# Kernel tuning notes

Measured on AMD Instinct MI355X. Metric: run time of the kernel, lower is better.

Reference implementation:

```python
import jax, jax.numpy as jnp
import numpy as np

N_CLASSES = 2  # FS-MOL binary labels


def setup_inputs() -> dict:
    key = jax.random.key(0)
    k1, k2, k3 = jax.random.split(key, 3)
    Ns, Nq, d = 512, 16384, 512
    support_features = jax.random.normal(k1, (Ns, d), dtype=jnp.float32)
    support_labels = jax.random.randint(k2, (Ns,), 0, N_CLASSES, dtype=jnp.int64)
    query_features = jax.random.normal(k3, (Nq, d), dtype=jnp.float32)
    return {
        "support_features": support_features,
        "support_labels": support_labels,
        "query_features": query_features,
    }


def _cov(x):
    # rowvar=False covariance of [N, d] -> [d, d], matching _estimate_cov
    xc = x - jnp.mean(x, axis=0, keepdims=True)
    return (xc.T @ xc) / (x.shape[0] - 1)


def reference(support_features, support_labels, query_features):
    d = support_features.shape[1]
    dt = support_features.dtype
    task_cov = _cov(support_features)          # [d, d]
    reg = jnp.asarray(0.1, dt) * jnp.eye(d, dtype=dt)

    def per_class(c):
        mask = (support_labels == c).astype(dt)            # [Ns]
        n = mask.sum()                                      # scalar count
        mean = (mask[:, None] * support_features).sum(0) / n
        xc = (support_features - mean) * mask[:, None]      # zero out other classes
        cov_c = (xc.T @ xc) / (n - 1.0)
        lam = jnp.minimum(n / (n + 1.0), jnp.asarray(0.1, dt))
        prec = jnp.linalg.inv(lam * cov_c + (1.0 - lam) * task_cov + reg)
        return mean, prec

    means, precs = jax.vmap(per_class)(jnp.arange(N_CLASSES))  # [C,d], [C,d,d]

    # Mahalanobis: diff[c,q,:] = mean_c - query_q  (matches repeated_class_means - repeated_target)
    diff = means[:, None, :] - query_features[None, :, :]      # [C, Nq, d]
    h = jnp.einsum('cqd,cde->cqe', diff, precs)                # [C, Nq, d]
    logits = -(h * diff).sum(-1).T                             # [Nq, C]
    return logits
```

## Files before the change

### kernel.cpp

```cpp
#include <hip/hip_runtime.h>

#define NS 512
#define DF 512
#define NQ 16384

#define WS_MEAN0 0
#define WS_MEAN1 512
#define WS_MEANA 1024
#define WS_CNT   1536
#define WS_V0    2048
#define WS_V1    2560
#define WS_KC    3072
#define WS_M     4096
#define WS_PB    (WS_M + 2*DF*DF)
#define WS_QB    (WS_PB + DF*DF)
#define WS_GP    WS_QB

typedef __attribute__((ext_vector_type(8))) short short8;
typedef __attribute__((ext_vector_type(4))) float floatx4;

__device__ __forceinline__ unsigned short f2bf(float f) {
    unsigned u = __float_as_uint(f);
    unsigned r = (u + 0x7fffu + ((u >> 16) & 1u)) >> 16;
    return (unsigned short)r;
}

__device__ __forceinline__ float readlane_f(float v, int lane) {
    return __uint_as_float(__builtin_amdgcn_readlane(__float_as_uint(v), lane));
}

__device__ __forceinline__ void load_lds16(const void* g, void* l) {
    __builtin_amdgcn_global_load_lds(
        (const __attribute__((address_space(1))) unsigned int*)g,
        (__attribute__((address_space(3))) unsigned int*)l, 16, 0, 0);
}

__global__ __launch_bounds__(512) void k_stats(const float* __restrict__ S,
                                               const int* __restrict__ lab,
                                               float* __restrict__ ws) {
    __shared__ int lb[NS];
    __shared__ float r0[8][64], r1[8][64];
    __shared__ int rc[8];
    int tid = threadIdx.x;
    for (int l = tid; l < NS; l += 512) lb[l] = lab[l];
    __syncthreads();
    int dl = tid & 63, ch = tid >> 6;
    int dd = blockIdx.x * 64 + dl;
    float s0 = 0.f, s1 = 0.f;
    int n1 = 0;
    for (int n = ch * 64; n < ch * 64 + 64; ++n) {
        float v = S[n * DF + dd];
        if (lb[n]) { s1 += v; n1++; } else { s0 += v; }
    }
    r0[ch][dl] = s0; r1[ch][dl] = s1;
    if (dl == 0) rc[ch] = n1;
    __syncthreads();
    if (ch == 0) {
        float t0 = 0.f, t1 = 0.f; int n1t = 0;
#pragma unroll
        for (int x = 0; x < 8; ++x) { t0 += r0[x][dl]; t1 += r1[x][dl]; n1t += rc[x]; }
        float fn1 = (float)n1t, fn0 = (float)(NS - n1t);
        ws[WS_MEAN0 + dd] = t0 / fn0;
        ws[WS_MEAN1 + dd] = t1 / fn1;
        ws[WS_MEANA + dd] = (t0 + t1) / (float)NS;
        if (blockIdx.x == 0 && dl == 0) {
            ws[WS_CNT] = fn0; ws[WS_CNT + 1] = fn1;
            ws[WS_KC] = 0.f; ws[WS_KC + 1] = 0.f;
        }
    }
}

__global__ __launch_bounds__(256) void k_gram_part(const float* __restrict__ S,
                                                   const int* __restrict__ lab,
                                                   float* __restrict__ ws) {
    __shared__ float SA[16 * 65];
    __shared__ float SB[16 * 65];
    __shared__ int lb[16];
    int tx = threadIdx.x, ty = threadIdx.y;
    int tid = ty * 16 + tx;
    int i0 = blockIdx.x * 64, j0 = blockIdx.y * 64;
    int z = blockIdx.z;
    float a0[4][4] = {{0.f}}, a1[4][4] = {{0.f}};
    for (int nc = z * 64; nc < z * 64 + 64; nc += 16) {
#pragma unroll
        for (int l = 0; l < 4; ++l) {
            int idx = tid + 256 * l;
            int nn = idx >> 6, col = idx & 63;
            SA[nn * 65 + col] = S[(nc + nn) * DF + i0 + col];
            SB[nn * 65 + col] = S[(nc + nn) * DF + j0 + col];
        }
        if (tid < 16) lb[tid] = lab[nc + tid];
        __syncthreads();
#pragma unroll
        for (int kk = 0; kk < 16; ++kk) {
            float av[4], bv[4];
#pragma unroll
            for (int r = 0; r < 4; ++r) av[r] = SA[kk * 65 + ty * 4 + r];
#pragma unroll
            for (int s = 0; s < 4; ++s) bv[s] = SB[kk * 65 + tx * 4 + s];
            if (lb[kk]) {
#pragma unroll
                for (int r = 0; r < 4; ++r)
#pragma unroll
                    for (int s = 0; s < 4; ++s) a1[r][s] += av[r] * bv[s];
            } else {
#pragma unroll
                for (int r = 0; r < 4; ++r)
#pragma unroll
                    for (int s = 0; s < 4; ++s) a0[r][s] += av[r] * bv[s];
            }
        }
        __syncthreads();
    }
    float* Gp = ws + WS_GP;
#pragma unroll
    for (int r = 0; r < 4; ++r) {
        int i = i0 + ty * 4 + r;
#pragma unroll
        for (int s = 0; s < 4; ++s) {
            int j = j0 + tx * 4 + s;
            Gp[((z * 2 + 0) * DF + i) * DF + j] = a0[r][s];
            Gp[((z * 2 + 1) * DF + i) * DF + j] = a1[r][s];
        }
    }
}

__global__ __launch_bounds__(256) void k_asm(float* __restrict__ ws) {
    const float* Gp = ws + WS_GP;
    int e = blockIdx.x * 256 + threadIdx.x;
    int i = e >> 9, j = e & 511;
    float g0 = 0.f, g1 = 0.f;
#pragma unroll
    for (int ch = 0; ch < 8; ++ch) {
        g0 += Gp[((ch * 2 + 0) * DF + i) * DF + j];
        g1 += Gp[((ch * 2 + 1) * DF + i) * DF + j];
    }
    float n0 = ws[WS_CNT], n1 = ws[WS_CNT + 1];
    float lam0 = fminf(n0 / (n0 + 1.f), 0.1f);
    float lam1 = fminf(n1 / (n1 + 1.f), 0.1f);
    float m0i = ws[WS_MEAN0 + i], m1i = ws[WS_MEAN1 + i], mai = ws[WS_MEANA + i];
    float m0j = ws[WS_MEAN0 + j], m1j = ws[WS_MEAN1 + j], maj = ws[WS_MEANA + j];
    float task = (g0 + g1 - (float)NS * mai * maj) / (float)(NS - 1);
    float cov0 = (g0 - n0 * m0i * m0j) / (n0 - 1.f);
    float cov1 = (g1 - n1 * m1i * m1j) / (n1 - 1.f);
    float dg = (i == j) ? 0.1f : 0.f;
    ws[WS_M + i * DF + j] = lam0 * cov0 + (1.f - lam0) * task + dg;
    ws[WS_M + DF * DF + i * DF + j] = lam1 * cov1 + (1.f - lam1) * task + dg;
}

__global__ __launch_bounds__(512) void k_step(float* __restrict__ ws, int k, int wbf) {
    int c = blockIdx.y;
    int jh = blockIdx.z;
    int ti = blockIdx.x >> 3, tj = blockIdx.x & 7;
    float* Mb = ws + WS_M + c * DF * DF;
    float* Akk = Mb + (k * 64) * DF + k * 64;
    unsigned short* pb = (unsigned short*)(ws + WS_PB) + (size_t)c * DF * DF;
    __shared__ float T[64 * 66];
    __shared__ float LV[64 * 65];
    __shared__ float LU[64 * 34];
    __shared__ float D1[64 * 34];
    __shared__ float rbuf[2][4][64];
    int tid = threadIdx.x;
    int jl = tid & 63, w = tid >> 6;
    int w4 = w & 3;
    bool isdiag = (ti == k) && (tj == k);
    bool isrow = (ti == k) && (tj != k);
    bool iscol = (tj == k) && (ti != k);

#pragma unroll
    for (int m = 0; m < 8; ++m) {
        int idx = tid + 512 * m;
        int i = idx >> 6, j = idx & 63;
        T[i * 66 + j] = Akk[i * DF + j];
    }
    if (ti != k) {
        const float* src = Mb + (ti * 64) * DF + k * 64;
#pragma unroll
        for (int m = 0; m < 8; ++m) {
            int idx = tid + 512 * m;
            int i = idx >> 6, j = idx & 63;
            LV[i * 65 + j] = src[i * DF + j];
        }
    }
    if (tj != k) {
        const float* src = Mb + (k * 64) * DF + tj * 64 + jh * 32;
#pragma unroll
        for (int m = 0; m < 4; ++m) {
            int idx = tid + 512 * m;
            int i = idx >> 5, j = idx & 31;
            LU[i * 34 + j] = src[i * DF + j];
        }
    }
    __syncthreads();

    float Tr[16];
#pragma unroll
    for (int m = 0; m < 16; ++m) Tr[m] = T[(w4 * 16 + m) * 66 + jl];
#pragma unroll
    for (int r = 0; r < 16; ++r) {
        const int q0 = r * 4;
        const int par = r & 1;
        if (w == (q0 >> 4)) {
            const int mb = q0 & 15;
            rbuf[par][0][jl] = Tr[mb + 0];
            rbuf[par][1][jl] = Tr[mb + 1];
            rbuf[par][2][jl] = Tr[mb + 2];
            rbuf[par][3][jl] = Tr[mb + 3];
        }
        __syncthreads();
        float B[4][4];
#pragma unroll
        for (int a = 0; a < 4; ++a)
#pragma unroll
            for (int bb = 0; bb < 4; ++bb) B[a][bb] = rbuf[par][a][q0 + bb];
#pragma unroll
        for (int p = 0; p < 4; ++p) {
            float piv = 1.0f / B[p][p];
#pragma unroll
            for (int j = 0; j < 4; ++j) if (j != p) B[p][j] *= piv;
#pragma unroll
            for (int i = 0; i < 4; ++i) if (i != p) {
                float f = B[i][p];
#pragma unroll
                for (int j = 0; j < 4; ++j) if (j != p) B[i][j] -= f * B[p][j];
                B[i][p] = -f * piv;
            }
            B[p][p] = piv;
        }
        float r0v = rbuf[par][0][jl], r1v = rbuf[par][1][jl];
        float r2v = rbuf[par][2][jl], r3v = rbuf[par][3][jl];
        float nr[4];
#pragma unroll
        for (int a = 0; a < 4; ++a)
            nr[a] = B[a][0] * r0v + B[a][1] * r1v + B[a][2] * r2v + B[a][3] * r3v;
        bool colin = ((jl >> 2) == r);
        int bsel = jl & 3;
        float Bc[4];
#pragma unroll
        for (int a = 0; a < 4; ++a)
            Bc[a] = bsel == 0 ? B[a][0]
                  : (bsel == 1 ? B[a][1] : (bsel == 2 ? B[a][2] : B[a][3]));
#pragma unroll
        for (int m = 0; m < 16; ++m) {
            float cv0 = readlane_f(Tr[m], q0 + 0);
            float cv1 = readlane_f(Tr[m], q0 + 1);
            float cv2 = readlane_f(Tr[m], q0 + 2);
            float cv3 = readlane_f(Tr[m], q0 + 3);
            float g = Tr[m] - (cv0 * nr[0] + cv1 * nr[1] + cv2 * nr[2] + cv3 * nr[3]);
            bool rowin = (((w4 * 16 + m) >> 2) == r);
            float gcol = -(cv0 * Bc[0] + cv1 * Bc[1] + cv2 * Bc[2] + cv3 * Bc[3]);
            if (rowin) g = nr[m & 3];
            if (colin) g = rowin ? Bc[m & 3] : gcol;
            Tr[m] = g;
        }
    }
    if (w < 4) {
#pragma unroll
        for (int m = 0; m < 16; ++m) T[(w4 * 16 + m) * 66 + jl] = Tr[m];
    }
    __syncthreads();

    int tx16 = tid & 15, ty32 = tid >> 4;
    int cb0 = jh * 32;
    if (isdiag) {
#pragma unroll
        for (int m = 0; m < 4; ++m) {
            int idx = tid + 512 * m;
            int i = idx >> 5, j = idx & 31;
            float v = T[i * 66 + cb0 + j];
            Akk[i * DF + cb0 + j] = v;
            if (wbf) pb[(size_t)(k * 64 + i) * DF + k * 64 + cb0 + j] = f2bf(v);
        }
    } else if (isrow) {
        float acc[2][2] = {{0.f}};
#pragma unroll 8
        for (int kk = 0; kk < 64; ++kk) {
            float av0 = T[(ty32 * 2 + 0) * 66 + kk];
            float av1 = T[(ty32 * 2 + 1) * 66 + kk];
            float2 bv = *(const float2*)&LU[kk * 34 + tx16 * 2];
            acc[0][0] += av0 * bv.x; acc[0][1] += av0 * bv.y;
            acc[1][0] += av1 * bv.x; acc[1][1] += av1 * bv.y;
        }
        float* dst = Mb + (k * 64) * DF + tj * 64 + cb0;
#pragma unroll
        for (int r = 0; r < 2; ++r) {
            *(float2*)&dst[(ty32 * 2 + r) * DF + tx16 * 2] = make_float2(acc[r][0], acc[r][1]);
            if (wbf) {
                unsigned up = (unsigned)f2bf(acc[r][0]) | ((unsigned)f2bf(acc[r][1]) << 16);
                *(unsigned*)&pb[(size_t)(k * 64 + ty32 * 2 + r) * DF + tj * 64 + cb0 + tx16 * 2] = up;
            }
        }
    } else if (iscol) {
        float acc[2][2] = {{0.f}};
#pragma unroll 8
        for (int kk = 0; kk < 64; ++kk) {
            float av0 = LV[(ty32 * 2 + 0) * 65 + kk];
            float av1 = LV[(ty32 * 2 + 1) * 65 + kk];
            float2 bv = *(const float2*)&T[kk * 66 + cb0 + tx16 * 2];
            acc[0][0] += av0 * bv.x; acc[0][1] += av0 * bv.y;
            acc[1][0] += av1 * bv.x; acc[1][1] += av1 * bv.y;
        }
        float* dst = Mb + (ti * 64) * DF + k * 64 + cb0;
#pragma unroll
        for (int r = 0; r < 2; ++r) {
            float v0 = -acc[r][0], v1 = -acc[r][1];
            *(float2*)&dst[(ty32 * 2 + r) * DF + tx16 * 2] = make_float2(v0, v1);
            if (wbf) {
                unsigned up = (unsigned)f2bf(v0) | ((unsigned)f2bf(v1) << 16);
                *(unsigned*)&pb[(size_t)(ti * 64 + ty32 * 2 + r) * DF + k * 64 + cb0 + tx16 * 2] = up;
            }
        }
    } else {
        float a1[2][2] = {{0.f}};
#pragma unroll 8
        for (int kk = 0; kk < 64; ++kk) {
            float av0 = T[(ty32 * 2 + 0) * 66 + kk];
            float av1 = T[(ty32 * 2 + 1) * 66 + kk];
            float2 bv = *(const float2*)&LU[kk * 34 + tx16 * 2];
            a1[0][0] += av0 * bv.x; a1[0][1] += av0 * bv.y;
            a1[1][0] += av1 * bv.x; a1[1][1] += av1 * bv.y;
        }
        __syncthreads();
#pragma unroll
        for (int r = 0; r < 2; ++r)
            *(float2*)&D1[(ty32 * 2 + r) * 34 + tx16 * 2] = make_float2(a1[r][0], a1[r][1]);
        __syncthreads();
        float a2[2][2] = {{0.f}};
#pragma unroll 8
        for (int kk = 0; kk < 64; ++kk) {
            float av0 = LV[(ty32 * 2 + 0) * 65 + kk];
            float av1 = LV[(ty32 * 2 + 1) * 65 + kk];
            float2 bv = *(const float2*)&D1[kk * 34 + tx16 * 2];
            a2[0][0] += av0 * bv.x; a2[0][1] += av0 * bv.y;
            a2[1][0] += av1 * bv.x; a2[1][1] += av1 * bv.y;
        }
        float* dst = Mb + (ti * 64) * DF + tj * 64 + cb0;
#pragma unroll
        for (int r = 0; r < 2; ++r) {
            float2 old = *(const float2*)&dst[(ty32 * 2 + r) * DF + tx16 * 2];
            float nv0 = old.x - a2[r][0], nv1 = old.y - a2[r][1];
            *(float2*)&dst[(ty32 * 2 + r) * DF + tx16 * 2] = make_float2(nv0, nv1);
            if (wbf) {
                unsigned up = (unsigned)f2bf(nv0) | ((unsigned)f2bf(nv1) << 16);
                *(unsigned*)&pb[(size_t)(ti * 64 + ty32 * 2 + r) * DF + tj * 64 + cb0 + tx16 * 2] = up;
            }
        }
    }
}

__global__ __launch_bounds__(256) void k_vk(float* __restrict__ ws) {
    int c = blockIdx.x >> 3, rb = blockIdx.x & 7;
    const float* P = ws + WS_M + c * DF * DF;
    const float* mc = ws + (c ? WS_MEAN1 : WS_MEAN0);
    float* v = ws + (c ? WS_V1 : WS_V0);
    __shared__ float ml[DF];
    __shared__ float red[4][64];
    int tid = threadIdx.x;
    for (int l = tid; l < DF; l += 256) ml[l] = mc[l];
    __syncthreads();
    int rl = tid & 63, ch = tid >> 6;
    int row = rb * 64 + rl;
    float dot = 0.f;
    const float* pr = P + (size_t)row * DF + ch * 128;
    for (int t = 0; t < 32; ++t) {
        float4 pv = *(const float4*)(pr + t * 4);
        const float* mm = ml + ch * 128 + t * 4;
        dot += pv.x * mm[0] + pv.y * mm[1] + pv.z * mm[2] + pv.w * mm[3];
    }
    red[ch][rl] = dot;
    __syncthreads();
    if (ch == 0) {
        float d = red[0][rl] + red[1][rl] + red[2][rl] + red[3][rl];
        v[row] = d;
        float kp = d * ml[row];
#pragma unroll
        for (int off = 32; off > 0; off >>= 1) kp += __shfl_down(kp, off);
        if (rl == 0) atomicAdd(&ws[WS_KC + c], kp);
    }
}

__global__ __launch_bounds__(256) void k_qinit(const float* __restrict__ Q,
                                               float* __restrict__ ws,
                                               float* __restrict__ out) {
    unsigned short* qbw = (unsigned short*)(ws + WS_QB);
    const float* v0 = ws + WS_V0;
    const float* v1 = ws + WS_V1;
    int lane = threadIdx.x & 63;
    int q = blockIdx.x * 4 + (threadIdx.x >> 6);
    const float* qrow = Q + (size_t)q * DF + lane * 8;
    float4 x0 = *(const float4*)(qrow);
    float4 x1 = *(const float4*)(qrow + 4);
    const float* v0p = v0 + lane * 8;
    const float* v1p = v1 + lane * 8;
    float4 w00 = *(const float4*)(v0p), w01 = *(const float4*)(v0p + 4);
    float4 w10 = *(const float4*)(v1p), w11 = *(const float4*)(v1p + 4);
    float a0 = x0.x * w00.x + x0.y * w00.y + x0.z * w00.z + x0.w * w00.w
             + x1.x * w01.x + x1.y * w01.y + x1.z * w01.z + x1.w * w01.w;
    float a1 = x0.x * w10.x + x0.y * w10.y + x0.z * w10.z + x0.w * w10.w
             + x1.x * w11.x + x1.y * w11.y + x1.z * w11.z + x1.w * w11.w;
    short8 r;
    r[0] = (short)f2bf(x0.x); r[1] = (short)f2bf(x0.y);
    r[2] = (short)f2bf(x0.z); r[3] = (short)f2bf(x0.w);
    r[4] = (short)f2bf(x1.x); r[5] = (short)f2bf(x1.y);
    r[6] = (short)f2bf(x1.z); r[7] = (short)f2bf(x1.w);
    *(short8*)(qbw + (size_t)q * DF + lane * 8) = r;
#pragma unroll
    for (int off = 32; off > 0; off >>= 1) {
        a0 += __shfl_down(a0, off);
        a1 += __shfl_down(a1, off);
    }
    if (lane == 0) {
        out[q * 2 + 0] = 2.f * a0 - ws[WS_KC + 0];
        out[q * 2 + 1] = 2.f * a1 - ws[WS_KC + 1];
    }
}

__global__ __launch_bounds__(256, 3) void k_gemm(const float* __restrict__ ws,
                                                 float* __restrict__ out) {
    const unsigned short* qb = (const unsigned short*)(ws + WS_QB);
    int c = blockIdx.y >> 2;
    int n0 = (blockIdx.y & 3) * 128;
    const unsigned short* pbc = (const unsigned short*)(ws + WS_PB) + (size_t)c * DF * DF;
    int q0 = blockIdx.x * 128;
    __shared__ __align__(16) unsigned short Abuf[128 * 64];
    __shared__ __align__(16) unsigned short Bbuf[128 * 64];
    int tid = threadIdx.x;
    int w = tid >> 6, lane = tid & 63;
    int quad = lane >> 4, l15 = lane & 15;
    floatx4 acc[2][8];
#pragma unroll
    for (int mt = 0; mt < 2; ++mt)
#pragma unroll
        for (int nt = 0; nt < 8; ++nt) acc[mt][nt] = (floatx4)(0.f);

    for (int kt = 0; kt < 8; ++kt) {
        int kc = kt * 64;
#pragma unroll
        for (int i = 0; i < 4; ++i) {
            int o = tid * 16 + i * 4096;
            int row = o >> 7;
            int sg = ((o >> 4) & 7) ^ (row & 7);
            load_lds16(qb + (size_t)(q0 + row) * DF + kc + sg * 8, (char*)Abuf + o);
        }
#pragma unroll
        for (int i = 0; i < 4; ++i) {
            int o = tid * 16 + i * 4096;
            int row = o >> 7;
            int sg = ((o >> 4) & 7) ^ (row & 7);
            load_lds16(pbc + (size_t)(n0 + row) * DF + kc + sg * 8, (char*)Bbuf + o);
        }
        __syncthreads();
#pragma unroll
        for (int kk2 = 0; kk2 < 2; ++kk2) {
            int u = ((kk2 * 4 + quad) ^ (l15 & 7)) << 4;
            short8 b[8];
#pragma unroll
            for (int nt = 0; nt < 8; ++nt)
                b[nt] = *(const short8*)((const char*)Bbuf + (nt * 16 + l15) * 128 + u);
#pragma unroll
            for (int mt = 0; mt < 2; ++mt) {
                short8 a = *(const short8*)((const char*)Abuf + (w * 32 + mt * 16 + l15) * 128 + u);
#pragma unroll
                for (int nt = 0; nt < 8; ++nt)
                    acc[mt][nt] = __builtin_amdgcn_mfma_f32_16x16x32_bf16(a, b[nt], acc[mt][nt], 0, 0, 0);
            }
        }
        __syncthreads();
    }
#pragma unroll
    for (int mt = 0; mt < 2; ++mt)
#pragma unroll
        for (int reg = 0; reg < 4; ++reg) {
            int row = w * 32 + mt * 16 + quad * 4 + reg;
            float part = 0.f;
#pragma unroll
            for (int nt = 0; nt < 8; ++nt) {
                float h = acc[mt][nt][reg];
                unsigned qu = qb[(size_t)(q0 + row) * DF + n0 + nt * 16 + l15];
                part += h * __uint_as_float(qu << 16);
            }
            part += __shfl_xor(part, 1);
            part += __shfl_xor(part, 2);
            part += __shfl_xor(part, 4);
            part += __shfl_xor(part, 8);
            if (l15 == 0) atomicAdd(&out[(size_t)(q0 + row) * 2 + c], -part);
        }
}

extern "C" void kernel_launch(void* const* d_in, const int* in_sizes, int n_in,
                              void* d_out, int out_size, void* d_ws, size_t ws_size,
                              hipStream_t stream) {
    const float* S = (const float*)d_in[0];
    const int* lab = (const int*)d_in[1];
    const float* Q = (const float*)d_in[2];
    float* out = (float*)d_out;
    float* ws = (float*)d_ws;

    k_stats<<<8, 512, 0, stream>>>(S, lab, ws);
    k_gram_part<<<dim3(8, 8, 8), dim3(16, 16), 0, stream>>>(S, lab, ws);
    k_asm<<<1024, 256, 0, stream>>>(ws);
    for (int k = 0; k < 8; ++k)
        k_step<<<dim3(64, 2, 2), 512, 0, stream>>>(ws, k, k == 7 ? 1 : 0);
    k_vk<<<16, 256, 0, stream>>>(ws);
    k_qinit<<<NQ / 4, 256, 0, stream>>>(Q, ws, out);
    k_gemm<<<dim3(NQ / 128, 8), 256, 0, stream>>>(ws, out);
}
```

Measured before the change: 387.4 us.

## Split block Gauss-Jordan step into update kernels with lookahead pivot inversion

Each step of the blocked Gauss-Jordan inversion previously made every block redundantly invert the 64x64 pivot tile in LDS. Now the pivot inverse is computed once: k_pivot0 handles the first, and a dedicated block in k_updB inverts the next step's pivot from the freshly updated trailing tile, writing it to a double-buffered scratch area. The step is split into a trailing-update kernel followed by a row/column/diagonal kernel, and the stats and gram kernels are merged into one launch. This cuts the redundant serial inversion work per block but adds a kernel launch per step and changes the order of operations.

```diff
diff --git a/kernel.cpp b/kernel.cpp
--- a/kernel.cpp
+++ b/kernel.cpp
@@ -15,6 +15,7 @@
 #define WS_PB    (WS_M + 2*DF*DF)
 #define WS_QB    (WS_PB + DF*DF)
 #define WS_GP    WS_QB
+#define WS_SCR   WS_QB
 
 typedef __attribute__((ext_vector_type(8))) short short8;
 typedef __attribute__((ext_vector_type(4))) float floatx4;
@@ -35,51 +36,123 @@
         (__attribute__((address_space(3))) unsigned int*)l, 16, 0, 0);
 }
 
-__global__ __launch_bounds__(512) void k_stats(const float* __restrict__ S,
+__device__ __forceinline__ void gj_invert64(float* T, float (*rbuf)[4][64], int tid) {
+    int jl = tid & 63, w = tid >> 6;
+    float Tr[16];
+    if (w < 4) {
+#pragma unroll
+        for (int m = 0; m < 16; ++m) Tr[m] = T[(w * 16 + m) * 66 + jl];
+    }
+#pragma unroll
+    for (int r = 0; r < 16; ++r) {
+        const int q0 = r * 4;
+        const int par = r & 1;
+        if (w == (q0 >> 4)) {
+            const int mb = q0 & 15;
+            rbuf[par][0][jl] = Tr[mb + 0];
+            rbuf[par][1][jl] = Tr[mb + 1];
+            rbuf[par][2][jl] = Tr[mb + 2];
+            rbuf[par][3][jl] = Tr[mb + 3];
+        }
+        __syncthreads();
+        if (w < 4) {
+            float B[4][4];
+#pragma unroll
+            for (int a = 0; a < 4; ++a)
+#pragma unroll
+                for (int bb = 0; bb < 4; ++bb) B[a][bb] = rbuf[par][a][q0 + bb];
+#pragma unroll
+            for (int p = 0; p < 4; ++p) {
+                float piv = 1.0f / B[p][p];
+#pragma unroll
+                for (int j = 0; j < 4; ++j) if (j != p) B[p][j] *= piv;
+#pragma unroll
+                for (int i = 0; i < 4; ++i) if (i != p) {
+                    float f = B[i][p];
+#pragma unroll
+                    for (int j = 0; j < 4; ++j) if (j != p) B[i][j] -= f * B[p][j];
+                    B[i][p] = -f * piv;
+                }
+                B[p][p] = piv;
+            }
+            float r0v = rbuf[par][0][jl], r1v = rbuf[par][1][jl];
+            float r2v = rbuf[par][2][jl], r3v = rbuf[par][3][jl];
+            float nr[4];
+#pragma unroll
+            for (int a = 0; a < 4; ++a)
+                nr[a] = B[a][0] * r0v + B[a][1] * r1v + B[a][2] * r2v + B[a][3] * r3v;
+            bool colin = ((jl >> 2) == r);
+            int bsel = jl & 3;
+            float Bc[4];
+#pragma unroll
+            for (int a = 0; a < 4; ++a)
+                Bc[a] = bsel == 0 ? B[a][0]
+                      : (bsel == 1 ? B[a][1] : (bsel == 2 ? B[a][2] : B[a][3]));
+#pragma unroll
+            for (int m = 0; m < 16; ++m) {
+                float cv0 = readlane_f(Tr[m], q0 + 0);
+                float cv1 = readlane_f(Tr[m], q0 + 1);
+                float cv2 = readlane_f(Tr[m], q0 + 2);
+                float cv3 = readlane_f(Tr[m], q0 + 3);
+                float g = Tr[m] - (cv0 * nr[0] + cv1 * nr[1] + cv2 * nr[2] + cv3 * nr[3]);
+                bool rowin = (((w * 16 + m) >> 2) == r);
+                float gcol = -(cv0 * Bc[0] + cv1 * Bc[1] + cv2 * Bc[2] + cv3 * Bc[3]);
+                if (rowin) g = nr[m & 3];
+                if (colin) g = rowin ? Bc[m & 3] : gcol;
+                Tr[m] = g;
+            }
+        }
+    }
+    if (w < 4) {
+#pragma unroll
+        for (int m = 0; m < 16; ++m) T[(w * 16 + m) * 66 + jl] = Tr[m];
+    }
+    __syncthreads();
+}
+
+__global__ __launch_bounds__(256) void k_front(const float* __restrict__ S,
                                                const int* __restrict__ lab,
                                                float* __restrict__ ws) {
-    __shared__ int lb[NS];
-    __shared__ float r0[8][64], r1[8][64];
-    __shared__ int rc[8];
-    int tid = threadIdx.x;
-    for (int l = tid; l < NS; l += 512) lb[l] = lab[l];
-    __syncthreads();
-    int dl = tid & 63, ch = tid >> 6;
-    int dd = blockIdx.x * 64 + dl;
-    float s0 = 0.f, s1 = 0.f;
-    int n1 = 0;
-    for (int n = ch * 64; n < ch * 64 + 64; ++n) {
-        float v = S[n * DF + dd];
-        if (lb[n]) { s1 += v; n1++; } else { s0 += v; }
-    }
-    r0[ch][dl] = s0; r1[ch][dl] = s1;
-    if (dl == 0) rc[ch] = n1;
-    __syncthreads();
-    if (ch == 0) {
-        float t0 = 0.f, t1 = 0.f; int n1t = 0;
-#pragma unroll
-        for (int x = 0; x < 8; ++x) { t0 += r0[x][dl]; t1 += r1[x][dl]; n1t += rc[x]; }
-        float fn1 = (float)n1t, fn0 = (float)(NS - n1t);
-        ws[WS_MEAN0 + dd] = t0 / fn0;
-        ws[WS_MEAN1 + dd] = t1 / fn1;
-        ws[WS_MEANA + dd] = (t0 + t1) / (float)NS;
-        if (blockIdx.x == 0 && dl == 0) {
-            ws[WS_CNT] = fn0; ws[WS_CNT + 1] = fn1;
-            ws[WS_KC] = 0.f; ws[WS_KC + 1] = 0.f;
-        }
-    }
-}
-
-__global__ __launch_bounds__(256) void k_gram_part(const float* __restrict__ S,
-                                                   const int* __restrict__ lab,
-                                                   float* __restrict__ ws) {
+    int b = blockIdx.x, tid = threadIdx.x;
+    if (b >= 512) {
+        __shared__ int slb[NS];
+        __shared__ float r0[4][64], r1[4][64];
+        __shared__ int rc[4];
+        int bs = b - 512;
+        for (int l = tid; l < NS; l += 256) slb[l] = lab[l];
+        __syncthreads();
+        int dl = tid & 63, ch = tid >> 6;
+        int dd = bs * 64 + dl;
+        float s0 = 0.f, s1 = 0.f;
+        int n1 = 0;
+        for (int n = ch * 128; n < ch * 128 + 128; ++n) {
+            float v = S[n * DF + dd];
+            if (slb[n]) { s1 += v; n1++; } else { s0 += v; }
+        }
+        r0[ch][dl] = s0; r1[ch][dl] = s1;
+        if (dl == 0) rc[ch] = n1;
+        __syncthreads();
+        if (ch == 0) {
+            float t0 = 0.f, t1 = 0.f; int n1t = 0;
+#pragma unroll
+            for (int x = 0; x < 4; ++x) { t0 += r0[x][dl]; t1 += r1[x][dl]; n1t += rc[x]; }
+            float fn1 = (float)n1t, fn0 = (float)(NS - n1t);
+            ws[WS_MEAN0 + dd] = t0 / fn0;
+            ws[WS_MEAN1 + dd] = t1 / fn1;
+            ws[WS_MEANA + dd] = (t0 + t1) / (float)NS;
+            if (bs == 0 && dl == 0) {
+                ws[WS_CNT] = fn0; ws[WS_CNT + 1] = fn1;
+                ws[WS_KC] = 0.f; ws[WS_KC + 1] = 0.f;
+            }
+        }
+        return;
+    }
     __shared__ float SA[16 * 65];
     __shared__ float SB[16 * 65];
     __shared__ int lb[16];
-    int tx = threadIdx.x, ty = threadIdx.y;
-    int tid = ty * 16 + tx;
-    int i0 = blockIdx.x * 64, j0 = blockIdx.y * 64;
-    int z = blockIdx.z;
+    int tx = tid & 15, ty = tid >> 4;
+    int i0 = (b & 7) * 64, j0 = ((b >> 3) & 7) * 64;
+    int z = b >> 6;
     float a0[4][4] = {{0.f}}, a1[4][4] = {{0.f}};
     for (int nc = z * 64; nc < z * 64 + 64; nc += 16) {
 #pragma unroll
@@ -148,32 +221,48 @@
     ws[WS_M + DF * DF + i * DF + j] = lam1 * cov1 + (1.f - lam1) * task + dg;
 }
 
-__global__ __launch_bounds__(512) void k_step(float* __restrict__ ws, int k, int wbf) {
-    int c = blockIdx.y;
-    int jh = blockIdx.z;
+__global__ __launch_bounds__(256) void k_pivot0(float* __restrict__ ws) {
+    int c = blockIdx.x;
+    __shared__ float T[64 * 66];
+    __shared__ float rbuf[2][4][64];
+    const float* Akk = ws + WS_M + (size_t)c * DF * DF;
+    int tid = threadIdx.x;
+#pragma unroll
+    for (int m = 0; m < 16; ++m) {
+        int idx = tid + 256 * m;
+        int i = idx >> 6, j = idx & 63;
+        T[i * 66 + j] = Akk[i * DF + j];
+    }
+    __syncthreads();
+    gj_invert64(T, rbuf, tid);
+    float* scr = ws + WS_SCR + (0 * 2 + c) * 4096;
+#pragma unroll
+    for (int m = 0; m < 16; ++m) {
+        int idx = tid + 256 * m;
+        int i = idx >> 6, j = idx & 63;
+        scr[i * 64 + j] = T[i * 66 + j];
+    }
+}
+
+__global__ __launch_bounds__(512) void k_updA(float* __restrict__ ws, int k, int wbf) {
+    int c = blockIdx.y, jh = blockIdx.z;
     int ti = blockIdx.x >> 3, tj = blockIdx.x & 7;
-    float* Mb = ws + WS_M + c * DF * DF;
-    float* Akk = Mb + (k * 64) * DF + k * 64;
+    if (ti == k || tj == k) return;
+    float* Mb = ws + WS_M + (size_t)c * DF * DF;
     unsigned short* pb = (unsigned short*)(ws + WS_PB) + (size_t)c * DF * DF;
+    const float* scr_in = ws + WS_SCR + ((k & 1) * 2 + c) * 4096;
+    int tid = threadIdx.x;
     __shared__ float T[64 * 66];
     __shared__ float LV[64 * 65];
     __shared__ float LU[64 * 34];
     __shared__ float D1[64 * 34];
-    __shared__ float rbuf[2][4][64];
-    int tid = threadIdx.x;
-    int jl = tid & 63, w = tid >> 6;
-    int w4 = w & 3;
-    bool isdiag = (ti == k) && (tj == k);
-    bool isrow = (ti == k) && (tj != k);
-    bool iscol = (tj == k) && (ti != k);
-
 #pragma unroll
     for (int m = 0; m < 8; ++m) {
         int idx = tid + 512 * m;
         int i = idx >> 6, j = idx & 63;
-        T[i * 66 + j] = Akk[i * DF + j];
-    }
-    if (ti != k) {
+        T[i * 66 + j] = scr_in[i * 64 + j];
+    }
+    {
         const float* src = Mb + (ti * 64) * DF + k * 64;
 #pragma unroll
         for (int m = 0; m < 8; ++m) {
@@ -182,7 +271,7 @@
             LV[i * 65 + j] = src[i * DF + j];
         }
     }
-    if (tj != k) {
+    {
         const float* src = Mb + (k * 64) * DF + tj * 64 + jh * 32;
 #pragma unroll
         for (int m = 0; m < 4; ++m) {
@@ -192,92 +281,111 @@
         }
     }
     __syncthreads();
-
-    float Tr[16];
-#pragma unroll
-    for (int m = 0; m < 16; ++m) Tr[m] = T[(w4 * 16 + m) * 66 + jl];
-#pragma unroll
-    for (int r = 0; r < 16; ++r) {
-        const int q0 = r * 4;
-        const int par = r & 1;
-        if (w == (q0 >> 4)) {
-            const int mb = q0 & 15;
-            rbuf[par][0][jl] = Tr[mb + 0];
-            rbuf[par][1][jl] = Tr[mb + 1];
-            rbuf[par][2][jl] = Tr[mb + 2];
-            rbuf[par][3][jl] = Tr[mb + 3];
-        }
-        __syncthreads();
-        float B[4][4];
-#pragma unroll
-        for (int a = 0; a < 4; ++a)
-#pragma unroll
-            for (int bb = 0; bb < 4; ++bb) B[a][bb] = rbuf[par][a][q0 + bb];
-#pragma unroll
-        for (int p = 0; p < 4; ++p) {
-            float piv = 1.0f / B[p][p];
-#pragma unroll
-            for (int j = 0; j < 4; ++j) if (j != p) B[p][j] *= piv;
-#pragma unroll
-            for (int i = 0; i < 4; ++i) if (i != p) {
-                float f = B[i][p];
-#pragma unroll
-                for (int j = 0; j < 4; ++j) if (j != p) B[i][j] -= f * B[p][j];
-                B[i][p] = -f * piv;
-            }
-            B[p][p] = piv;
-        }
-        float r0v = rbuf[par][0][jl], r1v = rbuf[par][1][jl];
-        float r2v = rbuf[par][2][jl], r3v = rbuf[par][3][jl];
-        float nr[4];
-#pragma unroll
-        for (int a = 0; a < 4; ++a)
-            nr[a] = B[a][0] * r0v + B[a][1] * r1v + B[a][2] * r2v + B[a][3] * r3v;
-        bool colin = ((jl >> 2) == r);
-        int bsel = jl & 3;
-        float Bc[4];
-#pragma unroll
-        for (int a = 0; a < 4; ++a)
-            Bc[a] = bsel == 0 ? B[a][0]
-                  : (bsel == 1 ? B[a][1] : (bsel == 2 ? B[a][2] : B[a][3]));
-#pragma unroll
-        for (int m = 0; m < 16; ++m) {
-            float cv0 = readlane_f(Tr[m], q0 + 0);
-            float cv1 = readlane_f(Tr[m], q0 + 1);
-            float cv2 = readlane_f(Tr[m], q0 + 2);
-            float cv3 = readlane_f(Tr[m], q0 + 3);
-            float g = Tr[m] - (cv0 * nr[0] + cv1 * nr[1] + cv2 * nr[2] + cv3 * nr[3]);
-            bool rowin = (((w4 * 16 + m) >> 2) == r);
-            float gcol = -(cv0 * Bc[0] + cv1 * Bc[1] + cv2 * Bc[2] + cv3 * Bc[3]);
-            if (rowin) g = nr[m & 3];
-            if (colin) g = rowin ? Bc[m & 3] : gcol;
-            Tr[m] = g;
-        }
-    }
-    if (w < 4) {
-#pragma unroll
-        for (int m = 0; m < 16; ++m) T[(w4 * 16 + m) * 66 + jl] = Tr[m];
-    }
-    __syncthreads();
-
     int tx16 = tid & 15, ty32 = tid >> 4;
     int cb0 = jh * 32;
-    if (isdiag) {
-#pragma unroll
-        for (int m = 0; m < 4; ++m) {
+    float a1[2][2] = {{0.f}};
+#pragma unroll 8
+    for (int kk = 0; kk < 64; ++kk) {
+        float av0 = T[(ty32 * 2 + 0) * 66 + kk];
+        float av1 = T[(ty32 * 2 + 1) * 66 + kk];
+        float2 bv = *(const float2*)&LU[kk * 34 + tx16 * 2];
+        a1[0][0] += av0 * bv.x; a1[0][1] += av0 * bv.y;
+        a1[1][0] += av1 * bv.x; a1[1][1] += av1 * bv.y;
+    }
+#pragma unroll
+    for (int r = 0; r < 2; ++r)
+        *(float2*)&D1[(ty32 * 2 + r) * 34 + tx16 * 2] = make_float2(a1[r][0], a1[r][1]);
+    __syncthreads();
+    float a2[2][2] = {{0.f}};
+#pragma unroll 8
+    for (int kk = 0; kk < 64; ++kk) {
+        float av0 = LV[(ty32 * 2 + 0) * 65 + kk];
+        float av1 = LV[(ty32 * 2 + 1) * 65 + kk];
+        float2 bv = *(const float2*)&D1[kk * 34 + tx16 * 2];
+        a2[0][0] += av0 * bv.x; a2[0][1] += av0 * bv.y;
+        a2[1][0] += av1 * bv.x; a2[1][1] += av1 * bv.y;
+    }
+    float* dst = Mb + (ti * 64) * DF + tj * 64 + cb0;
+#pragma unroll
+    for (int r = 0; r < 2; ++r) {
+        float2 old = *(const float2*)&dst[(ty32 * 2 + r) * DF + tx16 * 2];
+        float nv0 = old.x - a2[r][0], nv1 = old.y - a2[r][1];
+        *(float2*)&dst[(ty32 * 2 + r) * DF + tx16 * 2] = make_float2(nv0, nv1);
+        if (wbf) {
+            unsigned up = (unsigned)f2bf(nv0) | ((unsigned)f2bf(nv1) << 16);
+            *(unsigned*)&pb[(size_t)(ti * 64 + ty32 * 2 + r) * DF + tj * 64 + cb0 + tx16 * 2] = up;
+        }
+    }
+}
+
+__global__ __launch_bounds__(512) void k_updB(float* __restrict__ ws, int k, int wbf) {
+    int c = blockIdx.y, jh = blockIdx.z;
+    int x = blockIdx.x;
+    int tid = threadIdx.x;
+    __shared__ float T[64 * 66];
+    __shared__ float X[64 * 65];
+    float* Mb = ws + WS_M + (size_t)c * DF * DF;
+    unsigned short* pb = (unsigned short*)(ws + WS_PB) + (size_t)c * DF * DF;
+    const float* scr_in = ws + WS_SCR + ((k & 1) * 2 + c) * 4096;
+
+    if (x == 16) {
+        if (jh == 1 || k == 7) return;
+        const float* src = Mb + ((k + 1) * 64) * DF + (k + 1) * 64;
+#pragma unroll
+        for (int m = 0; m < 8; ++m) {
             int idx = tid + 512 * m;
-            int i = idx >> 5, j = idx & 31;
-            float v = T[i * 66 + cb0 + j];
-            Akk[i * DF + cb0 + j] = v;
-            if (wbf) pb[(size_t)(k * 64 + i) * DF + k * 64 + cb0 + j] = f2bf(v);
-        }
-    } else if (isrow) {
+            int i = idx >> 6, j = idx & 63;
+            T[i * 66 + j] = src[i * DF + j];
+        }
+        __syncthreads();
+        gj_invert64(T, (float(*)[4][64])X, tid);
+        float* scr_out = ws + WS_SCR + (((k + 1) & 1) * 2 + c) * 4096;
+#pragma unroll
+        for (int m = 0; m < 8; ++m) {
+            int idx = tid + 512 * m;
+            int i = idx >> 6, j = idx & 63;
+            scr_out[i * 64 + j] = T[i * 66 + j];
+        }
+        return;
+    }
+    int cb0 = jh * 32;
+    int tx16 = tid & 15, ty32 = tid >> 4;
+    if (x < 8) {
+        int tj = x;
+        if (tj == k) {
+            float* Akk = Mb + (k * 64) * DF + k * 64;
+#pragma unroll
+            for (int m = 0; m < 4; ++m) {
+                int idx = tid + 512 * m;
+                int i = idx >> 5, j = idx & 31;
+                float v = scr_in[i * 64 + cb0 + j];
+                Akk[i * DF + cb0 + j] = v;
+                if (wbf) pb[(size_t)(k * 64 + i) * DF + k * 64 + cb0 + j] = f2bf(v);
+            }
+            return;
+        }
+#pragma unroll
+        for (int m = 0; m < 8; ++m) {
+            int idx = tid + 512 * m;
+            int i = idx >> 6, j = idx & 63;
+            T[i * 66 + j] = scr_in[i * 64 + j];
+        }
+        {
+            const float* src = Mb + (k * 64) * DF + tj * 64 + cb0;
+#pragma unroll
+            for (int m = 0; m < 4; ++m) {
+                int idx = tid + 512 * m;
+                int i = idx >> 5, j = idx & 31;
+                X[i * 34 + j] = src[i * DF + j];
+            }
+        }
+        __syncthreads();
         float acc[2][2] = {{0.f}};
 #pragma unroll 8
         for (int kk = 0; kk < 64; ++kk) {
             float av0 = T[(ty32 * 2 + 0) * 66 + kk];
             float av1 = T[(ty32 * 2 + 1) * 66 + kk];
-            float2 bv = *(const float2*)&LU[kk * 34 + tx16 * 2];
+            float2 bv = *(const float2*)&X[kk * 34 + tx16 * 2];
             acc[0][0] += av0 * bv.x; acc[0][1] += av0 * bv.y;
             acc[1][0] += av1 * bv.x; acc[1][1] += av1 * bv.y;
         }
@@ -290,67 +398,60 @@
                 *(unsigned*)&pb[(size_t)(k * 64 + ty32 * 2 + r) * DF + tj * 64 + cb0 + tx16 * 2] = up;
             }
         }
-    } else if (iscol) {
-        float acc[2][2] = {{0.f}};
-#pragma unroll 8
+    } else {
+        int ti = x - 8;
+        if (ti == k || jh == 1) return;
+#pragma unroll
+        for (int m = 0; m < 8; ++m) {
+            int idx = tid + 512 * m;
+            int i = idx >> 6, j = idx & 63;
+            T[i * 66 + j] = scr_in[i * 64 + j];
+        }
+        {
+            const float* src = Mb + (ti * 64) * DF + k * 64;
+#pragma unroll
+            for (int m = 0; m < 8; ++m) {
+                int idx = tid + 512 * m;
+                int i = idx >> 6, j = idx & 63;
+                X[i * 65 + j] = src[i * DF + j];
+            }
+        }
+        __syncthreads();
+        float acc[2][2][2];
+#pragma unroll
+        for (int p = 0; p < 2; ++p)
+#pragma unroll
+            for (int r = 0; r < 2; ++r) { acc[p][r][0] = 0.f; acc[p][r][1] = 0.f; }
+#pragma unroll 4
         for (int kk = 0; kk < 64; ++kk) {
-            float av0 = LV[(ty32 * 2 + 0) * 65 + kk];
-            float av1 = LV[(ty32 * 2 + 1) * 65 + kk];
-            float2 bv = *(const float2*)&T[kk * 66 + cb0 + tx16 * 2];
-            acc[0][0] += av0 * bv.x; acc[0][1] += av0 * bv.y;
-            acc[1][0] += av1 * bv.x; acc[1][1] += av1 * bv.y;
-        }
-        float* dst = Mb + (ti * 64) * DF + k * 64 + cb0;
-#pragma unroll
-        for (int r = 0; r < 2; ++r) {
-            float v0 = -acc[r][0], v1 = -acc[r][1];
-            *(float2*)&dst[(ty32 * 2 + r) * DF + tx16 * 2] = make_float2(v0, v1);
-            if (wbf) {
-                unsigned up = (unsigned)f2bf(v0) | ((unsigned)f2bf(v1) << 16);
-                *(unsigned*)&pb[(size_t)(ti * 64 + ty32 * 2 + r) * DF + k * 64 + cb0 + tx16 * 2] = up;
-            }
-        }
-    } else {
-        float a1[2][2] = {{0.f}};
-#pragma unroll 8
-        for (int kk = 0; kk < 64; ++kk) {
-            float av0 = T[(ty32 * 2 + 0) * 66 + kk];
-            float av1 = T[(ty32 * 2 + 1) * 66 + kk];
-            float2 bv = *(const float2*)&LU[kk * 34 + tx16 * 2];
-            a1[0][0] += av0 * bv.x; a1[0][1] += av0 * bv.y;
-            a1[1][0] += av1 * bv.x; a1[1][1] += av1 * bv.y;
-        }
-        __syncthreads();
-#pragma unroll
-        for (int r = 0; r < 2; ++r)
-            *(float2*)&D1[(ty32 * 2 + r) * 34 + tx16 * 2] = make_float2(a1[r][0], a1[r][1]);
-        __syncthreads();
-        float a2[2][2] = {{0.f}};
-#pragma unroll 8
-        for (int kk = 0; kk < 64; ++kk) {
-            float av0 = LV[(ty32 * 2 + 0) * 65 + kk];
-            float av1 = LV[(ty32 * 2 + 1) * 65 + kk];
-            float2 bv = *(const float2*)&D1[kk * 34 + tx16 * 2];
-            a2[0][0] += av0 * bv.x; a2[0][1] += av0 * bv.y;
-            a2[1][0] += av1 * bv.x; a2[1][1] += av1 * bv.y;
-        }
-        float* dst = Mb + (ti * 64) * DF + tj * 64 + cb0;
-#pragma unroll
-        for (int r = 0; r < 2; ++r) {
-            float2 old = *(const float2*)&dst[(ty32 * 2 + r) * DF + tx16 * 2];
-            float nv0 = old.x - a2[r][0], nv1 = old.y - a2[r][1];
-            *(float2*)&dst[(ty32 * 2 + r) * DF + tx16 * 2] = make_float2(nv0, nv1);
-            if (wbf) {
-                unsigned up = (unsigned)f2bf(nv0) | ((unsigned)f2bf(nv1) << 16);
-                *(unsigned*)&pb[(size_t)(ti * 64 + ty32 * 2 + r) * DF + tj * 64 + cb0 + tx16 * 2] = up;
-            }
-        }
+            float av0 = X[(ty32 * 2 + 0) * 65 + kk];
+            float av1 = X[(ty32 * 2 + 1) * 65 + kk];
+            float2 b0 = *(const float2*)&T[kk * 66 + tx16 * 2];
+            float2 b1 = *(const float2*)&T[kk * 66 + 32 + tx16 * 2];
+            acc[0][0][0] += av0 * b0.x; acc[0][0][1] += av0 * b0.y;
+            acc[0][1][0] += av1 * b0.x; acc[0][1][1] += av1 * b0.y;
+            acc[1][0][0] += av0 * b1.x; acc[1][0][1] += av0 * b1.y;
+            acc[1][1][0] += av1 * b1.x; acc[1][1][1] += av1 * b1.y;
+        }
+        float* dst = Mb + (ti * 64) * DF + k * 64;
+#pragma unroll
+        for (int p = 0; p < 2; ++p)
+#pragma unroll
+            for (int r = 0; r < 2; ++r) {
+                int row = ty32 * 2 + r, col = p * 32 + tx16 * 2;
+                float v0 = -acc[p][r][0], v1 = -acc[p][r][1];
+                *(float2*)&dst[row * DF + col] = make_float2(v0, v1);
+                if (wbf) {
+                    unsigned up = (unsigned)f2bf(v0) | ((unsigned)f2bf(v1) << 16);
+                    *(unsigned*)&pb[(size_t)(ti * 64 + row) * DF + k * 64 + col] = up;
+                }
+            }
     }
 }
 
 __global__ __launch_bounds__(256) void k_vk(float* __restrict__ ws) {
     int c = blockIdx.x >> 3, rb = blockIdx.x & 7;
-    const float* P = ws + WS_M + c * DF * DF;
+    const float* P = ws + WS_M + (size_t)c * DF * DF;
     const float* mc = ws + (c ? WS_MEAN1 : WS_MEAN0);
     float* v = ws + (c ? WS_V1 : WS_V0);
     __shared__ float ml[DF];
@@ -434,20 +535,20 @@
         for (int nt = 0; nt < 8; ++nt) acc[mt][nt] = (floatx4)(0.f);
 
     for (int kt = 0; kt < 8; ++kt) {
-        int kc = kt * 64;
+        int kc2 = kt * 64;
 #pragma unroll
         for (int i = 0; i < 4; ++i) {
             int o = tid * 16 + i * 4096;
             int row = o >> 7;
             int sg = ((o >> 4) & 7) ^ (row & 7);
-            load_lds16(qb + (size_t)(q0 + row) * DF + kc + sg * 8, (char*)Abuf + o);
+            load_lds16(qb + (size_t)(q0 + row) * DF + kc2 + sg * 8, (char*)Abuf + o);
         }
 #pragma unroll
         for (int i = 0; i < 4; ++i) {
             int o = tid * 16 + i * 4096;
             int row = o >> 7;
             int sg = ((o >> 4) & 7) ^ (row & 7);
-            load_lds16(pbc + (size_t)(n0 + row) * DF + kc + sg * 8, (char*)Bbuf + o);
+            load_lds16(pbc + (size_t)(n0 + row) * DF + kc2 + sg * 8, (char*)Bbuf + o);
         }
         __syncthreads();
 #pragma unroll
@@ -496,11 +597,14 @@
     float* out = (float*)d_out;
     float* ws = (float*)d_ws;
 
-    k_stats<<<8, 512, 0, stream>>>(S, lab, ws);
-    k_gram_part<<<dim3(8, 8, 8), dim3(16, 16), 0, stream>>>(S, lab, ws);
+    k_front<<<520, 256, 0, stream>>>(S, lab, ws);
     k_asm<<<1024, 256, 0, stream>>>(ws);
-    for (int k = 0; k < 8; ++k)
-        k_step<<<dim3(64, 2, 2), 512, 0, stream>>>(ws, k, k == 7 ? 1 : 0);
+    k_pivot0<<<2, 256, 0, stream>>>(ws);
+    for (int k = 0; k < 8; ++k) {
+        int wbf = (k == 7) ? 1 : 0;
+        k_updA<<<dim3(64, 2, 2), 512, 0, stream>>>(ws, k, wbf);
+        k_updB<<<dim3(17, 2, 2), 512, 0, stream>>>(ws, k, wbf);
+    }
     k_vk<<<16, 256, 0, stream>>>(ws);
     k_qinit<<<NQ / 4, 256, 0, stream>>>(Q, ws, out);
     k_gemm<<<dim3(NQ / 128, 8), 256, 0, stream>>>(ws, out);
```

Measured after the change: 353.3 us. 1.1x faster.
